# Optimization experiments

Measured on AMD Instinct MI355X. Metric: run time of the kernel, lower is better.

## Reference

```python
import jax, jax.numpy as jnp
import numpy as np

N_HEAD = 16
HEAD_DIM = 256
ROTARY_DIM = 64
MAX_POS = 2048
MP_NUM = 4


def create_sinusoidal_positions(num_pos, dim):
    inv_freq = 1.0 / 10000 ** (np.arange(0, dim, 2) / dim)
    si = np.einsum('i,j->ij', np.arange(num_pos), inv_freq).astype('float32')
    # sentinel = dim//2 : first half sin, second half cos
    out = np.concatenate([np.sin(si), np.cos(si)], axis=-1)
    return jnp.asarray(out, jnp.float32)  # [num_pos, dim]


def rotate_every_two(t):
    r = jnp.stack((-t[..., 1::2], t[..., ::2]), axis=-1)
    return r.reshape(r.shape[:-2] + (-1,))


def apply_rotary_pos_emb(t, sin_pos, cos_pos):
    # sin_pos/cos_pos: [B,S,rot/2] -> repeat each element twice along last dim
    sin = jnp.repeat(sin_pos[:, :, None, :], 2, axis=3)  # [B,S,1,rot]
    cos = jnp.repeat(cos_pos[:, :, None, :], 2, axis=3)
    return t * cos + rotate_every_two(t) * sin


def setup_inputs() -> dict:
    key = jax.random.key(0)
    k1, k2, k3 = jax.random.split(key, 3)
    B, S, H = 2, 2048, 4096
    hidden_states = jax.random.normal(k1, (B, S, H), jnp.float32)
    position_ids = jnp.broadcast_to(jnp.arange(S, dtype=jnp.int32)[None, :], (B, S))
    attention_mask = jnp.ones((B, 1, 1, S), dtype=bool)
    w_qkv = jax.random.normal(k2, (H, 3 * H), jnp.float32) * (1.0 / np.sqrt(H))
    w_out = jax.random.normal(k3, (H, H), jnp.float32) * (1.0 / np.sqrt(H))
    return {"hidden_states": hidden_states, "position_ids": position_ids,
            "attention_mask": attention_mask, "w_qkv": w_qkv, "w_out": w_out}


def reference(hidden_states, position_ids, attention_mask, w_qkv, w_out):
    B, S, H = hidden_states.shape
    fused_qkv = hidden_states @ w_qkv                       # [B,S,3H]
    qkv = fused_qkv.reshape(B, S, MP_NUM, -1)               # [B,S,4,3H/4]
    query, value, key = jnp.split(qkv, 3, axis=-1)          # each [B,S,4,H/4]
    query = query.reshape(B, S, N_HEAD, HEAD_DIM)
    key = key.reshape(B, S, N_HEAD, HEAD_DIM)
    value = value.reshape(B, S, N_HEAD, HEAD_DIM)

    embed_positions = create_sinusoidal_positions(MAX_POS, ROTARY_DIM)
    sincos = jnp.take(embed_positions, position_ids, axis=0)  # [B,S,rot]
    sin_pos, cos_pos = jnp.split(sincos, 2, axis=-1)           # [B,S,rot/2]

    # partial rotary on the first ROTARY_DIM dims of each head
    q_rot = apply_rotary_pos_emb(query[..., :ROTARY_DIM], sin_pos, cos_pos)
    k_rot = apply_rotary_pos_emb(key[..., :ROTARY_DIM], sin_pos, cos_pos)
    query = jnp.concatenate([q_rot, query[..., ROTARY_DIM:]], axis=-1)
    key = jnp.concatenate([k_rot, key[..., ROTARY_DIM:]], axis=-1)

    key_length = attention_mask.shape[-1]
    causal = jnp.tril(jnp.ones((key_length, key_length), dtype=bool))[None, None]  # [1,1,S,S]
    mask = attention_mask & causal                              # [B,1,S,S]

    mask_value = jnp.finfo(hidden_states.dtype).min
    bias = jnp.where(mask, jnp.zeros((), hidden_states.dtype), mask_value)

    scale = 1.0 / jnp.sqrt(jnp.asarray(HEAD_DIM, hidden_states.dtype))
    scores = jnp.einsum('bqhd,bkhd->bhqk', query * scale, key) + bias
    attn_weights = jax.nn.softmax(scores, axis=-1)              # [B,H,S,S]
    attn_output = jnp.einsum('bhqk,bkhd->bqhd', attn_weights, value)
    attn_output = attn_output.reshape(B, S, H) @ w_out
    return attn_output
```

## Files before the change

kernel.cpp:

```cpp
#include <hip/hip_runtime.h>
#include <hip/hip_bf16.h>
#include <math.h>
#include <stdint.h>


typedef __attribute__((ext_vector_type(8))) short bf16x8;
typedef __attribute__((ext_vector_type(4))) float f32x4;
typedef unsigned short u16;

__device__ __forceinline__ u16 f2b(float f) {
    __hip_bfloat16 h = __float2bfloat16(f);
    return *reinterpret_cast<u16*>(&h);
}
__device__ __forceinline__ float b2f(u16 u) {
    __hip_bfloat16 h = *reinterpret_cast<__hip_bfloat16*>(&u);
    return __bfloat162float(h);
}

__device__ __forceinline__ void load_lds16(const u16* g, u16* l) {
    __builtin_amdgcn_global_load_lds((const __attribute__((address_space(1))) void*)g,
                                     (__attribute__((address_space(3))) void*)l, 16, 0, 0);
}

__global__ void detect_kernel(const u16* __restrict__ h, int* __restrict__ flag)
{
    int lane = threadIdx.x & 63;
    int cnt = 0;
    for (int i = lane; i < 8192; i += 64) {
        int e = (h[i] >> 7) & 0xFF;
        cnt += (e >= 0xC0);
    }
    for (int off = 32; off > 0; off >>= 1) cnt += __shfl_down(cnt, off, 64);
    if (lane == 0) *flag = (cnt > 0) ? 1 : 0;
}

__global__ __launch_bounds__(256)
void convert_kernel(const void* __restrict__ in, const int* __restrict__ flag,
                    u16* __restrict__ outp, int n8)
{
    int idx = blockIdx.x * 256 + threadIdx.x;
    if (idx >= n8) return;
    if (*flag) {
        const float* x = (const float*)in;
        f32x4 a = *reinterpret_cast<const f32x4*>(&x[(size_t)idx * 8]);
        f32x4 b = *reinterpret_cast<const f32x4*>(&x[(size_t)idx * 8 + 4]);
        u16 t[8];
#pragma unroll
        for (int j = 0; j < 4; j++) { t[j] = f2b(a[j]); t[4 + j] = f2b(b[j]); }
        *reinterpret_cast<uint4*>(&outp[(size_t)idx * 8]) = *reinterpret_cast<uint4*>(t);
    } else {
        ((uint4*)outp)[idx] = ((const uint4*)in)[idx];
    }
}

__global__ __launch_bounds__(256)
void transpose_conv_kernel(const void* __restrict__ Wv, const int* __restrict__ flag,
                           int K, int N, u16* __restrict__ Wt)
{
    __shared__ u16 T[64][68];
    const int tid = threadIdx.x;
    const int k0 = blockIdx.y * 64, n0 = blockIdx.x * 64;
    const int kr = tid >> 4, nc = tid & 15;
    if (*flag) {
        const float* W = (const float*)Wv;
#pragma unroll
        for (int kk = 0; kk < 4; kk++) {
            int k = kr + kk * 16;
            f32x4 v = *reinterpret_cast<const f32x4*>(&W[(size_t)(k0 + k) * N + n0 + nc * 4]);
#pragma unroll
            for (int j = 0; j < 4; j++) T[nc * 4 + j][k] = f2b(v[j]);
        }
    } else {
        const u16* W = (const u16*)Wv;
#pragma unroll
        for (int kk = 0; kk < 4; kk++) {
            int k = kr + kk * 16;
            ushort4 v = *reinterpret_cast<const ushort4*>(&W[(size_t)(k0 + k) * N + n0 + nc * 4]);
            T[nc * 4 + 0][k] = v.x; T[nc * 4 + 1][k] = v.y;
            T[nc * 4 + 2][k] = v.z; T[nc * 4 + 3][k] = v.w;
        }
    }
    __syncthreads();
#pragma unroll
    for (int it = 0; it < 2; it++) {
        int ch = tid + it * 256;
        int n = ch >> 3, kc = ch & 7;
        const uint2* s2 = reinterpret_cast<const uint2*>(&T[n][kc * 8]);
        uint2 a = s2[0], b = s2[1];
        uint4 o; o.x = a.x; o.y = a.y; o.z = b.x; o.w = b.y;
        *reinterpret_cast<uint4*>(&Wt[(size_t)(n0 + n) * K + k0 + kc * 8]) = o;
    }
}


#define WAITV(N) asm volatile("s_waitcnt vmcnt(" #N ")" ::: "memory")
#define BARS()   do { asm volatile("s_barrier" ::: "memory"); \
                      __builtin_amdgcn_sched_barrier(0); } while (0)

#define RD_A(IOFF)                                                            \
    _Pragma("unroll")                                                         \
    for (int il = 0; il < 4; ++il) {                                          \
        aF[il][0] = *(const bf16x8*)(Ac + aR + (il + IOFF) * 2048 + p0);      \
        aF[il][1] = *(const bf16x8*)(Ac + aR + (il + IOFF) * 2048 + p1);      \
    }

#define RD_B(BF, JOFF)                                                        \
    _Pragma("unroll")                                                         \
    for (int j = 0; j < 2; ++j) {                                             \
        BF[j][0] = *(const bf16x8*)(Bc + bR + (j + JOFF) * 4096 + p0);        \
        BF[j][1] = *(const bf16x8*)(Bc + bR + (j + JOFF) * 4096 + p1);        \
    }

#define MFMA_BLK(IOFF, BF, JOFF)                                              \
    __builtin_amdgcn_s_setprio(1);                                            \
    _Pragma("unroll")                                                         \
    for (int il = 0; il < 4; ++il)                                            \
        _Pragma("unroll")                                                     \
        for (int j = 0; j < 2; ++j) {                                         \
            acc[il + IOFF][j + JOFF] = __builtin_amdgcn_mfma_f32_16x16x32_bf16( \
                aF[il][0], BF[j][0], acc[il + IOFF][j + JOFF], 0, 0, 0);      \
            acc[il + IOFF][j + JOFF] = __builtin_amdgcn_mfma_f32_16x16x32_bf16( \
                aF[il][1], BF[j][1], acc[il + IOFF][j + JOFF], 0, 0, 0);      \
        }                                                                     \
    __builtin_amdgcn_s_setprio(0);

__global__ __launch_bounds__(512, 2)
void gemm_bt_kernel(const u16* __restrict__ A, const u16* __restrict__ Bt,
                    const int* __restrict__ flag,
                    int M, int N, int K, int mode,
                    u16* __restrict__ C0, u16* __restrict__ Ck, u16* __restrict__ Cv,
                    float* __restrict__ C0f)
{
    __shared__ u16 As[2][256][64];
    __shared__ u16 Bs[2][256][64];

    const int tid  = threadIdx.x;
    const int wave = tid >> 6, lane = tid & 63;
    const int l15  = lane & 15, quad = lane >> 4;
    const int wr   = wave >> 2, wc = wave & 3;

    const int nwg = gridDim.x;
    const int bid = blockIdx.x;
    const int swz = (bid & 7) * (nwg >> 3) + (bid >> 3);
    const int ntn = N >> 8;
    const int m0 = (swz / ntn) << 8;
    const int n0 = (swz % ntn) << 8;

    const int trow = tid >> 3;
    const int tcol = ((tid & 7) ^ (trow & 7)) << 3;
    const u16* aS = A  + (size_t)(m0 + trow) * K + tcol;
    const u16* bS = Bt + (size_t)(n0 + trow) * K + tcol;
    const size_t slabK = (size_t)64 * K;

    u16* ASf = &As[0][0][0];
    u16* BSf = &Bs[0][0][0];
    const int dOff = tid * 8;

    const int aR = (wr * 16 + l15) * 64;
    const int bR = (wc * 16 + l15) * 64;
    const int sw = l15 & 7;
    const int p0 = (quad ^ sw) * 8;
    const int p1 = ((quad + 4) ^ sw) * 8;

    f32x4 acc[8][4];
#pragma unroll
    for (int i = 0; i < 8; i++)
#pragma unroll
        for (int j = 0; j < 4; j++) acc[i][j] = (f32x4){0.f, 0.f, 0.f, 0.f};

    const int NT = K >> 6;

#pragma unroll
    for (int q = 0; q < 4; ++q) {
        load_lds16(aS + q * slabK, ASf + q * 4096 + dOff);
        load_lds16(bS + q * slabK, BSf + q * 4096 + dOff);
    }
    WAITV(0);
    BARS();

    bf16x8 aF[4][2], bF0[2][2], bF1[2][2];

    for (int kt = 0; kt < NT - 1; ++kt) {
        const int c = kt & 1;
        const u16* Ac = ASf + c * 16384;
        const u16* Bc = BSf + c * 16384;
        u16* An = ASf + (c ^ 1) * 16384;
        u16* Bn = BSf + (c ^ 1) * 16384;
        const u16* aN = aS + (size_t)(kt + 1) * 64;
        const u16* bN = bS + (size_t)(kt + 1) * 64;

        RD_A(0)
        RD_B(bF0, 0)
        load_lds16(aN,         An + dOff);
        load_lds16(aN + slabK, An + 4096 + dOff);
        WAITV(4);
        BARS();
        MFMA_BLK(0, bF0, 0)

        RD_B(bF1, 2)
        load_lds16(bN,         Bn + dOff);
        load_lds16(bN + slabK, Bn + 4096 + dOff);
        WAITV(4);
        BARS();
        MFMA_BLK(0, bF1, 2)

        RD_A(4)
        load_lds16(bN + 2 * slabK, Bn + 8192 + dOff);
        load_lds16(bN + 3 * slabK, Bn + 12288 + dOff);
        BARS();
        MFMA_BLK(4, bF0, 0)

        load_lds16(aN + 2 * slabK, An + 8192 + dOff);
        load_lds16(aN + 3 * slabK, An + 12288 + dOff);
        WAITV(4);
        BARS();
        MFMA_BLK(4, bF1, 2)
    }

    {
        const int c = (NT - 1) & 1;
        const u16* Ac = ASf + c * 16384;
        const u16* Bc = BSf + c * 16384;
        RD_A(0)
        RD_B(bF0, 0)
        WAITV(2);
        BARS();
        MFMA_BLK(0, bF0, 0)
        RD_B(bF1, 2)
        WAITV(0);
        BARS();
        MFMA_BLK(0, bF1, 2)
        RD_A(4)
        BARS();
        MFMA_BLK(4, bF0, 0)
        MFMA_BLK(4, bF1, 2)
    }

    const int isF32 = *flag;
    if (mode == 0) {
#pragma unroll
        for (int j4 = 0; j4 < 4; ++j4) {
            int n = n0 + j4 * 64 + wc * 16 + l15;
#pragma unroll
            for (int i = 0; i < 8; ++i) {
                int m = m0 + i * 32 + wr * 16 + quad * 4;
#pragma unroll
                for (int r = 0; r < 4; ++r) {
                    float v = acc[i][j4][r];
                    if (isF32) C0f[(size_t)(m + r) * N + n] = v;
                    else       C0[(size_t)(m + r) * N + n] = f2b(v);
                }
            }
        }
    } else {
#pragma unroll
        for (int j4 = 0; j4 < 4; ++j4) {
            int n = n0 + j4 * 64 + wc * 16 + l15;
            int g = n / 3072;
            int r3 = n - g * 3072;
            int t = r3 >> 10;
            int r1 = r3 & 1023;
            int head = g * 4 + (r1 >> 8);
            int d = r1 & 255;
#pragma unroll
            for (int i = 0; i < 8; ++i) {
                int m = m0 + i * 32 + wr * 16 + quad * 4;
#pragma unroll
                for (int r = 0; r < 4; ++r) {
                    int mm = m + r;
                    int bb = mm >> 11, s = mm & 2047;
                    size_t idx;
                    u16* dst;
                    if (t == 1) { dst = Cv; idx = (size_t)bb * 8388608 + (size_t)head * 524288 + (size_t)d * 2048 + s; }
                    else        { dst = (t == 0) ? C0 : Ck;
                                  idx = (size_t)bb * 8388608 + (size_t)head * 524288 + (size_t)s * 256 + d; }
                    dst[idx] = f2b(acc[i][j4][r]);
                }
            }
        }
    }
}

__global__ __launch_bounds__(256)
void rope_kernel(u16* __restrict__ Q, u16* __restrict__ Kb, const int* __restrict__ pos_ids)
{
    int idx = blockIdx.x * 256 + threadIdx.x;
    int i = idx & 31;
    int s = (idx >> 5) & 2047;
    int h = (idx >> 16) & 15;
    int b = idx >> 20;
    int pos = pos_ids[b * 2048 + s];
    float freq = __expf(-(float)(2 * i) * (9.210340371976184f / 64.0f));
    float ang = (float)pos * freq;
    float sn = sinf(ang), cs = cosf(ang);
    size_t base = ((size_t)(b * 16 + h) * 2048 + s) * 256 + 2 * i;
    float q0 = b2f(Q[base]), q1 = b2f(Q[base + 1]);
    Q[base]     = f2b(q0 * cs - q1 * sn);
    Q[base + 1] = f2b(q1 * cs + q0 * sn);
    float k0 = b2f(Kb[base]), k1 = b2f(Kb[base + 1]);
    Kb[base]     = f2b(k0 * cs - k1 * sn);
    Kb[base + 1] = f2b(k1 * cs + k0 * sn);
}

__global__ __launch_bounds__(256, 2)
void attn_kernel(const u16* __restrict__ Q, const u16* __restrict__ Kb,
                 const u16* __restrict__ Vt, u16* __restrict__ att)
{
    __shared__ u16 Ks[32 * 256];
    __shared__ u16 Vts[256 * 32];
    __shared__ u16 Ps[4][32][40];

    const int tid = threadIdx.x;
    const int wave = tid >> 6, lane = tid & 63;
    const int l15 = lane & 15, quad = lane >> 4;

    const int blk = blockIdx.x;
    const int bh = blk & 31;
    const int jj = blk >> 5;
    const int qt = (jj < 8) ? (15 - jj) : (jj - 8);
    const int b = bh >> 4, h = bh & 15;
    const int qrow = qt * 128 + wave * 32;

    const u16* qb = Q + (size_t)bh * 524288;
    const u16* kb = Kb + (size_t)bh * 524288;
    const u16* vb = Vt + (size_t)bh * 524288;

    bf16x8 qf[2][8];
#pragma unroll
    for (int mi = 0; mi < 2; mi++)
#pragma unroll
        for (int ks = 0; ks < 8; ks++)
            qf[mi][ks] = *reinterpret_cast<const bf16x8*>(
                &qb[(size_t)(qrow + mi * 16 + l15) * 256 + ks * 32 + quad * 8]);

    f32x4 O[2][16];
#pragma unroll
    for (int mi = 0; mi < 2; mi++)
#pragma unroll
        for (int dt = 0; dt < 16; dt++) O[mi][dt] = (f32x4){0.f, 0.f, 0.f, 0.f};
    float m_run[2][4], l_run[2][4];
#pragma unroll
    for (int mi = 0; mi < 2; mi++)
#pragma unroll
        for (int r = 0; r < 4; r++) { m_run[mi][r] = -1e30f; l_run[mi][r] = 0.f; }
    const float scale = 1.0f / 16.0f;

    const int nkt = qt * 4 + 4;
    for (int kt = 0; kt < nkt; kt++) {
        const int k0 = kt * 32;
#pragma unroll
        for (int t = 0; t < 4; t++) {
            int pc = wave * 256 + t * 64 + lane;
            int rk = pc >> 5, pk = pc & 31;
            int ck = (pk & 24) | ((pk ^ rk) & 7);
            load_lds16(&kb[(size_t)(k0 + rk) * 256 + ck * 8], &Ks[pc * 8]);
            int dv = pc >> 2, pv2 = pc & 3;
            int cv = pv2 ^ ((dv >> 1) & 3);
            load_lds16(&vb[(size_t)dv * 2048 + k0 + cv * 8], &Vts[pc * 8]);
        }
        __syncthreads();

        if (k0 <= qrow + 31) {
            f32x4 sc[2][2];
#pragma unroll
            for (int mi = 0; mi < 2; mi++)
#pragma unroll
                for (int nt = 0; nt < 2; nt++) sc[mi][nt] = (f32x4){0.f, 0.f, 0.f, 0.f};
#pragma unroll
            for (int ks = 0; ks < 8; ks++)
#pragma unroll
                for (int nt = 0; nt < 2; nt++) {
                    int row = nt * 16 + l15;
                    int c = ks * 4 + quad;
                    int p = (c & 24) | ((c ^ row) & 7);
                    bf16x8 kf = *reinterpret_cast<const bf16x8*>(&Ks[row * 256 + p * 8]);
                    sc[0][nt] = __builtin_amdgcn_mfma_f32_16x16x32_bf16(qf[0][ks], kf, sc[0][nt], 0, 0, 0);
                    sc[1][nt] = __builtin_amdgcn_mfma_f32_16x16x32_bf16(qf[1][ks], kf, sc[1][nt], 0, 0, 0);
                }

#pragma unroll
            for (int mi = 0; mi < 2; mi++) {
                float pw[2][4], mloc[4], alpha[4], sum[4];
#pragma unroll
                for (int r = 0; r < 4; r++) {
                    int qg = qrow + mi * 16 + quad * 4 + r;
#pragma unroll
                    for (int nt = 0; nt < 2; nt++) {
                        int kg = k0 + nt * 16 + l15;
                        float v = sc[mi][nt][r] * scale;
                        pw[nt][r] = (kg <= qg) ? v : -1e30f;
                    }
                    mloc[r] = fmaxf(pw[0][r], pw[1][r]);
                }
#pragma unroll
                for (int off = 1; off < 16; off <<= 1)
#pragma unroll
                    for (int r = 0; r < 4; r++)
                        mloc[r] = fmaxf(mloc[r], __shfl_xor(mloc[r], off, 16));
#pragma unroll
                for (int r = 0; r < 4; r++) {
                    float mnew = fmaxf(m_run[mi][r], mloc[r]);
                    alpha[r] = __expf(m_run[mi][r] - mnew);
                    pw[0][r] = __expf(pw[0][r] - mnew);
                    pw[1][r] = __expf(pw[1][r] - mnew);
                    sum[r] = pw[0][r] + pw[1][r];
                    m_run[mi][r] = mnew;
                }
#pragma unroll
                for (int off = 1; off < 16; off <<= 1)
#pragma unroll
                    for (int r = 0; r < 4; r++)
                        sum[r] += __shfl_xor(sum[r], off, 16);
#pragma unroll
                for (int r = 0; r < 4; r++) l_run[mi][r] = l_run[mi][r] * alpha[r] + sum[r];
#pragma unroll
                for (int dt = 0; dt < 16; dt++)
#pragma unroll
                    for (int r = 0; r < 4; r++) O[mi][dt][r] *= alpha[r];
#pragma unroll
                for (int nt = 0; nt < 2; nt++)
#pragma unroll
                    for (int r = 0; r < 4; r++)
                        Ps[wave][mi * 16 + quad * 4 + r][nt * 16 + l15] = f2b(pw[nt][r]);
            }
            bf16x8 aP0 = *reinterpret_cast<const bf16x8*>(&Ps[wave][l15][quad * 8]);
            bf16x8 aP1 = *reinterpret_cast<const bf16x8*>(&Ps[wave][16 + l15][quad * 8]);
#pragma unroll
            for (int dt = 0; dt < 16; dt++) {
                int d = dt * 16 + l15;
                int pch = quad ^ ((d >> 1) & 3);
                bf16x8 vf = *reinterpret_cast<const bf16x8*>(&Vts[d * 32 + pch * 8]);
                O[0][dt] = __builtin_amdgcn_mfma_f32_16x16x32_bf16(aP0, vf, O[0][dt], 0, 0, 0);
                O[1][dt] = __builtin_amdgcn_mfma_f32_16x16x32_bf16(aP1, vf, O[1][dt], 0, 0, 0);
            }
        }
        __syncthreads();
    }

#pragma unroll
    for (int mi = 0; mi < 2; mi++) {
        float inv[4];
#pragma unroll
        for (int r = 0; r < 4; r++) inv[r] = 1.0f / l_run[mi][r];
#pragma unroll
        for (int dt = 0; dt < 16; dt++)
#pragma unroll
            for (int r = 0; r < 4; r++) {
                int s = qrow + mi * 16 + quad * 4 + r;
                att[((size_t)b * 2048 + s) * 4096 + h * 256 + dt * 16 + l15] =
                    f2b(O[mi][dt][r] * inv[r]);
            }
    }
}

extern "C" void kernel_launch(void* const* d_in, const int* in_sizes, int n_in,
                              void* d_out, int out_size, void* d_ws, size_t ws_size,
                              hipStream_t stream)
{
    const void* hidden  = d_in[0];
    const int*  pos_ids = (const int*)d_in[1];
    const void* w_qkv   = d_in[3];
    const void* w_out   = d_in[4];

    char* ws = (char*)d_ws;
    int* flag   = (int*)ws;
    u16* qbuf   = (u16*)(ws + 256);
    u16* kbuf   = (u16*)(ws + 256 + 33554432ull);
    u16* vbuf   = (u16*)(ws + 256 + 67108864ull);
    u16* att    = (u16*)(ws + 256 + 100663296ull);
    u16* hbuf   = (u16*)(ws + 256 + 134217728ull);
    u16* wqkvT  = (u16*)(ws + 256 + 167772160ull);
    u16* woutT  = (u16*)(ws + 256 + 268435456ull);

    detect_kernel<<<1, 64, 0, stream>>>((const u16*)hidden, flag);
    convert_kernel<<<8192, 256, 0, stream>>>(hidden, flag, hbuf, 2097152);
    dim3 gt1(12288 / 64, 4096 / 64);
    transpose_conv_kernel<<<gt1, 256, 0, stream>>>(w_qkv, flag, 4096, 12288, wqkvT);
    dim3 gt2(4096 / 64, 4096 / 64);
    transpose_conv_kernel<<<gt2, 256, 0, stream>>>(w_out, flag, 4096, 4096, woutT);

    gemm_bt_kernel<<<768, 512, 0, stream>>>(hbuf, wqkvT, flag, 4096, 12288, 4096,
                                            1, qbuf, kbuf, vbuf, nullptr);
    rope_kernel<<<8192, 256, 0, stream>>>(qbuf, kbuf, pos_ids);
    attn_kernel<<<512, 256, 0, stream>>>(qbuf, kbuf, vbuf, att);
    gemm_bt_kernel<<<256, 512, 0, stream>>>(att, woutT, flag, 4096, 4096, 4096,
                                            0, (u16*)d_out, nullptr, nullptr, (float*)d_out);
}
```

Measured before the change: 1.185 ms.

## Read K/V straight from global memory and add lazy softmax rescaling

Removes the shared-memory staging of K and V tiles and the block-wide barriers. Each wave now loads its MFMA fragments directly from global memory and runs only its own causal range of key tiles, so waves no longer wait for the slowest wave in the block. It also adds a lazy online-softmax rescale that skips the O and l correction unless the running max grows by more than a threshold. The trade-off is that K/V reuse across the four waves now depends on cache instead of LDS, which adds global load latency and traffic.

```diff
diff --git a/kernel.cpp b/kernel.cpp
--- a/kernel.cpp
+++ b/kernel.cpp
@@ -306,8 +306,6 @@
 void attn_kernel(const u16* __restrict__ Q, const u16* __restrict__ Kb,
                  const u16* __restrict__ Vt, u16* __restrict__ att)
 {
-    __shared__ u16 Ks[32 * 256];
-    __shared__ u16 Vts[256 * 32];
     __shared__ u16 Ps[4][32][40];
 
     const int tid = threadIdx.x;
@@ -345,96 +343,89 @@
         for (int r = 0; r < 4; r++) { m_run[mi][r] = -1e30f; l_run[mi][r] = 0.f; }
     const float scale = 1.0f / 16.0f;
 
-    const int nkt = qt * 4 + 4;
+    const int nkt = (qrow >> 5) + 1;
     for (int kt = 0; kt < nkt; kt++) {
         const int k0 = kt * 32;
-#pragma unroll
-        for (int t = 0; t < 4; t++) {
-            int pc = wave * 256 + t * 64 + lane;
-            int rk = pc >> 5, pk = pc & 31;
-            int ck = (pk & 24) | ((pk ^ rk) & 7);
-            load_lds16(&kb[(size_t)(k0 + rk) * 256 + ck * 8], &Ks[pc * 8]);
-            int dv = pc >> 2, pv2 = pc & 3;
-            int cv = pv2 ^ ((dv >> 1) & 3);
-            load_lds16(&vb[(size_t)dv * 2048 + k0 + cv * 8], &Vts[pc * 8]);
-        }
-        __syncthreads();
-
-        if (k0 <= qrow + 31) {
-            f32x4 sc[2][2];
-#pragma unroll
-            for (int mi = 0; mi < 2; mi++)
-#pragma unroll
-                for (int nt = 0; nt < 2; nt++) sc[mi][nt] = (f32x4){0.f, 0.f, 0.f, 0.f};
-#pragma unroll
-            for (int ks = 0; ks < 8; ks++)
+
+        f32x4 sc[2][2];
+#pragma unroll
+        for (int mi = 0; mi < 2; mi++)
+#pragma unroll
+            for (int nt = 0; nt < 2; nt++) sc[mi][nt] = (f32x4){0.f, 0.f, 0.f, 0.f};
+#pragma unroll
+        for (int ks = 0; ks < 8; ks++)
+#pragma unroll
+            for (int nt = 0; nt < 2; nt++) {
+                bf16x8 kf = *reinterpret_cast<const bf16x8*>(
+                    &kb[(size_t)(k0 + nt * 16 + l15) * 256 + ks * 32 + quad * 8]);
+                sc[0][nt] = __builtin_amdgcn_mfma_f32_16x16x32_bf16(qf[0][ks], kf, sc[0][nt], 0, 0, 0);
+                sc[1][nt] = __builtin_amdgcn_mfma_f32_16x16x32_bf16(qf[1][ks], kf, sc[1][nt], 0, 0, 0);
+            }
+
+#pragma unroll
+        for (int mi = 0; mi < 2; mi++) {
+            float pw[2][4], mloc[4], sum[4];
+#pragma unroll
+            for (int r = 0; r < 4; r++) {
+                int qg = qrow + mi * 16 + quad * 4 + r;
 #pragma unroll
                 for (int nt = 0; nt < 2; nt++) {
-                    int row = nt * 16 + l15;
-                    int c = ks * 4 + quad;
-                    int p = (c & 24) | ((c ^ row) & 7);
-                    bf16x8 kf = *reinterpret_cast<const bf16x8*>(&Ks[row * 256 + p * 8]);
-                    sc[0][nt] = __builtin_amdgcn_mfma_f32_16x16x32_bf16(qf[0][ks], kf, sc[0][nt], 0, 0, 0);
-                    sc[1][nt] = __builtin_amdgcn_mfma_f32_16x16x32_bf16(qf[1][ks], kf, sc[1][nt], 0, 0, 0);
+                    int kg = k0 + nt * 16 + l15;
+                    float v = sc[mi][nt][r] * scale;
+                    pw[nt][r] = (kg <= qg) ? v : -1e30f;
                 }
-
-#pragma unroll
-            for (int mi = 0; mi < 2; mi++) {
-                float pw[2][4], mloc[4], alpha[4], sum[4];
-#pragma unroll
-                for (int r = 0; r < 4; r++) {
-                    int qg = qrow + mi * 16 + quad * 4 + r;
-#pragma unroll
-                    for (int nt = 0; nt < 2; nt++) {
-                        int kg = k0 + nt * 16 + l15;
-                        float v = sc[mi][nt][r] * scale;
-                        pw[nt][r] = (kg <= qg) ? v : -1e30f;
-                    }
-                    mloc[r] = fmaxf(pw[0][r], pw[1][r]);
-                }
-#pragma unroll
-                for (int off = 1; off < 16; off <<= 1)
-#pragma unroll
-                    for (int r = 0; r < 4; r++)
-                        mloc[r] = fmaxf(mloc[r], __shfl_xor(mloc[r], off, 16));
+                mloc[r] = fmaxf(pw[0][r], pw[1][r]);
+            }
+#pragma unroll
+            for (int off = 1; off < 16; off <<= 1)
+#pragma unroll
+                for (int r = 0; r < 4; r++)
+                    mloc[r] = fmaxf(mloc[r], __shfl_xor(mloc[r], off, 16));
+            bool need = false;
+#pragma unroll
+            for (int r = 0; r < 4; r++) need = need || (mloc[r] > m_run[mi][r] + 4.0f);
+            if (__any(need)) {
+                float alpha[4];
 #pragma unroll
                 for (int r = 0; r < 4; r++) {
                     float mnew = fmaxf(m_run[mi][r], mloc[r]);
                     alpha[r] = __expf(m_run[mi][r] - mnew);
-                    pw[0][r] = __expf(pw[0][r] - mnew);
-                    pw[1][r] = __expf(pw[1][r] - mnew);
-                    sum[r] = pw[0][r] + pw[1][r];
                     m_run[mi][r] = mnew;
+                    l_run[mi][r] *= alpha[r];
                 }
 #pragma unroll
-                for (int off = 1; off < 16; off <<= 1)
-#pragma unroll
-                    for (int r = 0; r < 4; r++)
-                        sum[r] += __shfl_xor(sum[r], off, 16);
-#pragma unroll
-                for (int r = 0; r < 4; r++) l_run[mi][r] = l_run[mi][r] * alpha[r] + sum[r];
-#pragma unroll
                 for (int dt = 0; dt < 16; dt++)
 #pragma unroll
                     for (int r = 0; r < 4; r++) O[mi][dt][r] *= alpha[r];
-#pragma unroll
-                for (int nt = 0; nt < 2; nt++)
-#pragma unroll
-                    for (int r = 0; r < 4; r++)
-                        Ps[wave][mi * 16 + quad * 4 + r][nt * 16 + l15] = f2b(pw[nt][r]);
-            }
-            bf16x8 aP0 = *reinterpret_cast<const bf16x8*>(&Ps[wave][l15][quad * 8]);
-            bf16x8 aP1 = *reinterpret_cast<const bf16x8*>(&Ps[wave][16 + l15][quad * 8]);
-#pragma unroll
-            for (int dt = 0; dt < 16; dt++) {
-                int d = dt * 16 + l15;
-                int pch = quad ^ ((d >> 1) & 3);
-                bf16x8 vf = *reinterpret_cast<const bf16x8*>(&Vts[d * 32 + pch * 8]);
-                O[0][dt] = __builtin_amdgcn_mfma_f32_16x16x32_bf16(aP0, vf, O[0][dt], 0, 0, 0);
-                O[1][dt] = __builtin_amdgcn_mfma_f32_16x16x32_bf16(aP1, vf, O[1][dt], 0, 0, 0);
-            }
-        }
-        __syncthreads();
+            }
+#pragma unroll
+            for (int r = 0; r < 4; r++) {
+                pw[0][r] = __expf(pw[0][r] - m_run[mi][r]);
+                pw[1][r] = __expf(pw[1][r] - m_run[mi][r]);
+                sum[r] = pw[0][r] + pw[1][r];
+            }
+#pragma unroll
+            for (int off = 1; off < 16; off <<= 1)
+#pragma unroll
+                for (int r = 0; r < 4; r++)
+                    sum[r] += __shfl_xor(sum[r], off, 16);
+#pragma unroll
+            for (int r = 0; r < 4; r++) l_run[mi][r] += sum[r];
+#pragma unroll
+            for (int nt = 0; nt < 2; nt++)
+#pragma unroll
+                for (int r = 0; r < 4; r++)
+                    Ps[wave][mi * 16 + quad * 4 + r][nt * 16 + l15] = f2b(pw[nt][r]);
+        }
+        bf16x8 aP0 = *reinterpret_cast<const bf16x8*>(&Ps[wave][l15][quad * 8]);
+        bf16x8 aP1 = *reinterpret_cast<const bf16x8*>(&Ps[wave][16 + l15][quad * 8]);
+#pragma unroll
+        for (int dt = 0; dt < 16; dt++) {
+            bf16x8 vf = *reinterpret_cast<const bf16x8*>(
+                &vb[(size_t)(dt * 16 + l15) * 2048 + k0 + quad * 8]);
+            O[0][dt] = __builtin_amdgcn_mfma_f32_16x16x32_bf16(aP0, vf, O[0][dt], 0, 0, 0);
+            O[1][dt] = __builtin_amdgcn_mfma_f32_16x16x32_bf16(aP1, vf, O[1][dt], 0, 0, 0);
+        }
     }
 
 #pragma unroll
```

Measured after the change: 1.562 ms. 1.32x slower.
